# Kernel optimization log

Measured on AMD Instinct MI355X. Metric: run time of the kernel, lower is better.

Reference implementation:

```python
import jax, jax.numpy as jnp
import numpy as np

K = 3
STRIDE = 1
PAD = 1

def conv2d(x, w, b, stride, padding):
    out = jax.lax.conv_general_dilated(x, w, (stride, stride), [(padding, padding), (padding, padding)],
                                       dimension_numbers=('NCHW', 'OIHW', 'NCHW'))
    if b is not None:
        out = out + b[None, :, None, None]
    return out

def deform_conv2d(x, offset, mask, weight, stride, padding):
    # torchvision-style modulated deformable conv (offset_groups=1, groups=1)
    B, C, H, W = x.shape
    C2 = weight.shape[0]
    KK = K * K
    Hout, Wout = offset.shape[2], offset.shape[3]
    off = offset.reshape(B, KK, 2, Hout, Wout)  # (dy, dx) pairs per kernel tap
    ky = jnp.repeat(jnp.arange(K), K)  # kernel row per tap [KK]
    kx = jnp.tile(jnp.arange(K), K)    # kernel col per tap [KK]
    base_y = (jnp.arange(Hout) * stride - padding).astype(jnp.float32)
    base_x = (jnp.arange(Wout) * stride - padding).astype(jnp.float32)
    py = off[:, :, 0] + ky[None, :, None, None] + base_y[None, None, :, None]  # [B,KK,Hout,Wout]
    px = off[:, :, 1] + kx[None, :, None, None] + base_x[None, None, None, :]
    y0f = jnp.floor(py); x0f = jnp.floor(px)
    ly = py - y0f; lx = px - x0f
    y0 = y0f.astype(jnp.int32); x0 = x0f.astype(jnp.int32)
    xf = x.reshape(B, C, H * W)

    def corner(yi, xi, wgt):
        valid = (yi >= 0) & (yi < H) & (xi >= 0) & (xi < W)
        idx = (jnp.clip(yi, 0, H - 1) * W + jnp.clip(xi, 0, W - 1)).reshape(B, -1)  # [B, KK*Hout*Wout]
        v = jax.vmap(lambda xb, ib: xb[:, ib])(xf, idx)  # [B, C, KK*Hout*Wout]
        return v * (wgt * valid).reshape(B, 1, -1)

    val = (corner(y0, x0, (1.0 - ly) * (1.0 - lx))
           + corner(y0, x0 + 1, (1.0 - ly) * lx)
           + corner(y0 + 1, x0, ly * (1.0 - lx))
           + corner(y0 + 1, x0 + 1, ly * lx))
    val = val * mask.reshape(B, 1, -1)  # modulation per (tap, spatial)
    val = val.reshape(B, C, KK, Hout, Wout)
    out = jnp.einsum('bckhw,ock->bohw', val, weight.reshape(C2, C, KK))
    return out

def setup_inputs() -> dict:
    key = jax.random.key(0)
    ks = jax.random.split(key, 6)
    B, C1, C2, H, W = 8, 256, 256, 64, 64
    x = jax.random.normal(ks[0], (B, C1, H, W), jnp.float32)
    offset_w = jax.random.normal(ks[1], (2 * K * K, C1, K, K), jnp.float32) * 0.01
    offset_b = jax.random.normal(ks[2], (2 * K * K,), jnp.float32) * 0.5
    mod_w = jax.random.normal(ks[3], (K * K, C1, K, K), jnp.float32) * 0.01
    mod_b = jnp.zeros((K * K,), jnp.float32)
    reg_w = jax.random.normal(ks[4], (C2, C1, K, K), jnp.float32) * np.float32(1.0 / np.sqrt(C1 * K * K))
    return {"x": x, "offset_w": offset_w, "offset_b": offset_b, "mod_w": mod_w, "mod_b": mod_b, "reg_w": reg_w}

def reference(x, offset_w, offset_b, mod_w, mod_b, reg_w):
    h, w = x.shape[2], x.shape[3]
    max_offset = max(h, w) / 4.0
    offset = jnp.clip(conv2d(x, offset_w, offset_b, STRIDE, PAD), -max_offset, max_offset)
    modulator = jax.nn.sigmoid(conv2d(x, mod_w, mod_b, STRIDE, PAD))
    return deform_conv2d(x, offset, modulator, reg_w, STRIDE, PAD)
```

## Files before the change

### kernel.cpp

```cpp
#include <hip/hip_runtime.h>
#include <math.h>

#define BB 8
#define CIN 256
#define COUT 256
#define HH 64
#define WW 64
#define OCM 27
#define KTOT 2304
#define NKT 72

typedef unsigned int u32;
typedef unsigned short u16;
typedef _Float16 f16;

#define WS_XBF 0
#define WS_W2 16777216
#define WS_W2OM 17956864
#define WS_OFFMOD 18104320

__device__ __forceinline__ u16 f2h(float f) {
    f16 h = (f16)f;
    return __builtin_bit_cast(u16, h);
}

typedef __attribute__((address_space(1))) const unsigned int* gptr_t;
typedef __attribute__((address_space(3))) unsigned int* lptr_t;
__device__ __forceinline__ void gl2lds16(const void* g, void* l) {
    __builtin_amdgcn_global_load_lds((gptr_t)g, (lptr_t)l, 16, 0, 0);
}

typedef __attribute__((ext_vector_type(8))) f16 frag;
typedef __attribute__((ext_vector_type(2))) f16 h2;
typedef __attribute__((ext_vector_type(4))) float f4;

__device__ __forceinline__ int sw_off(int row, int oct) {
    return (row << 5) + ((oct ^ ((row >> 1) & 3)) << 3);
}

#define BARRIER_RAW() do { asm volatile("" ::: "memory"); \
    __builtin_amdgcn_s_barrier(); asm volatile("" ::: "memory"); } while (0)

__global__ __launch_bounds__(256) void k_prep(
    const float* __restrict__ x, const float* __restrict__ rw,
    const float* __restrict__ ow, const float* __restrict__ mw,
    u16* __restrict__ xbf, u16* __restrict__ w2, u16* __restrict__ w2om)
{
    const int bid = blockIdx.x;
    const int t = threadIdx.x;
    if (bid < 2048) {
        const int c0 = (bid & 3) << 6;
        const int y = (bid >> 2) & 63;
        const int b = bid >> 8;
        __shared__ float T[64][65];
        const int c = t >> 2, fi = t & 3;
        const float* xrow = x + (((size_t)(b * 256 + c0 + c)) << 12) + (y << 6);
#pragma unroll
        for (int k = 0; k < 4; ++k) {
            float4 v = *(const float4*)(xrow + ((fi + 4 * k) << 2));
            int w = (fi + 4 * k) << 2;
            T[c][w] = v.x; T[c][w + 1] = v.y; T[c][w + 2] = v.z; T[c][w + 3] = v.w;
        }
        __syncthreads();
        const int wl = t & 63, g = t >> 6;
        const int pr = wl & 31, wsub = wl >> 5;
        u32* xo = (u32*)xbf;
#pragma unroll
        for (int j = 0; j < 8; ++j) {
            int w = j * 8 + g * 2 + wsub;
            u32 v = (u32)f2h(T[2 * pr][w]) | ((u32)f2h(T[2 * pr + 1][w]) << 16);
            xo[((((size_t)b << 12) + (y << 6) + w) << 7) + (c0 >> 1) + pr] = v;
        }
    } else if (bid < 2336) {
        int o = ((bid - 2048) << 8) + t;
        int kk8 = (o & 3) << 3;
        int n = (o >> 2) & 255;
        int kt = o >> 10;
        u16 tmp[8];
#pragma unroll
        for (int j = 0; j < 8; ++j) {
            int k = kt * 32 + kk8 + j;
            int tap = k >> 8, c = k & 255;
            tmp[j] = f2h(rw[n * KTOT + c * 9 + tap]);
        }
        *(uint4*)&w2[((size_t)kt << 13) + (n << 5) + kk8] = *(uint4*)tmp;
    } else {
        int o = ((bid - 2336) << 8) + t;
        int kk8 = (o & 3) << 3;
        int oc = (o >> 2) & 31;
        int kt = o >> 7;
        u16 tmp[8];
#pragma unroll
        for (int j = 0; j < 8; ++j) {
            int k = kt * 32 + kk8 + j;
            int tap = k >> 8, c = k & 255;
            float v = 0.f;
            if (oc < 18) v = ow[oc * KTOT + c * 9 + tap];
            else if (oc < 27) v = mw[(oc - 18) * KTOT + c * 9 + tap];
            tmp[j] = f2h(v);
        }
        *(uint4*)&w2om[((size_t)kt << 10) + (oc << 5) + kk8] = *(uint4*)tmp;
    }
}

__global__ __launch_bounds__(512, 4) void k_offmod6(
    const u16* __restrict__ xbf, const u16* __restrict__ w2om,
    const float* __restrict__ ob, const float* __restrict__ mb,
    float* __restrict__ offmod)
{
    const int b = blockIdx.x & 7, h = blockIdx.x >> 3;
    const int t = threadIdx.x;
    const int lane = t & 63, wv = t >> 6;
    const int hf = wv >> 2;
    const int wl4 = wv & 3;
    const int th = t & 255;
    const int fr = lane & 15, q = lane >> 4;
    const int wm = wl4 << 4;
    const int mg = th >> 2, oct = th & 3;

    __shared__ u16 AsB[2][2][64 * 32];
    __shared__ u16 BsB[2][2][32 * 32];
    __shared__ float red[64][33];

    const u16* xb = xbf + ((size_t)b << 20);
    const int kbase = hf * 36;

    auto loadA = [&](int kt, uint4* r) {
        int tap = kt >> 3;
        int yy = h + tap / 3 - 1, xx = mg + tap % 3 - 1;
        int c0 = ((kt & 7) << 5) + (oct << 3);
        uint4 v = make_uint4(0, 0, 0, 0);
        if ((unsigned)yy < HH && (unsigned)xx < WW)
            v = *(const uint4*)(xb + (((size_t)yy << 6) + xx) * 256 + c0);
        *r = v;
    };
    auto loadB = [&](int kt, uint4* r) {
        if (th < 128) *r = *(const uint4*)(w2om + (size_t)kt * 1024 + (th >> 2) * 32 + (th & 3) * 8);
    };
    auto storeAB = [&](int buf, uint4* rA, uint4* rB) {
        *(uint4*)&AsB[hf][buf][sw_off(mg, oct)] = *rA;
        if (th < 128) *(uint4*)&BsB[hf][buf][sw_off(th >> 2, th & 3)] = *rB;
    };

    f4 acc[2];
    acc[0] = (f4){0.f, 0.f, 0.f, 0.f};
    acc[1] = (f4){0.f, 0.f, 0.f, 0.f};

    uint4 rA0, rB0, rA1, rB1;
    loadA(kbase, &rA0); loadB(kbase, &rB0);
    storeAB(0, &rA0, &rB0);
    loadA(kbase + 1, &rA1); loadB(kbase + 1, &rB1);
    asm volatile("s_waitcnt lgkmcnt(0)" ::: "memory");

    auto body = [&](int i, int p, uint4* cA, uint4* cB, uint4* nA, uint4* nB) {
        BARRIER_RAW();
        frag a  = *(const frag*)&AsB[hf][p][sw_off(wm + fr, q)];
        frag b0 = *(const frag*)&BsB[hf][p][sw_off(fr, q)];
        frag b1 = *(const frag*)&BsB[hf][p][sw_off(16 + fr, q)];
        if (i + 2 < 36) { loadA(kbase + i + 2, nA); loadB(kbase + i + 2, nB); }
        if (i + 1 < 36) storeAB(1 - p, cA, cB);
        acc[0] = __builtin_amdgcn_mfma_f32_16x16x32_f16(a, b0, acc[0], 0, 0, 0);
        acc[1] = __builtin_amdgcn_mfma_f32_16x16x32_f16(a, b1, acc[1], 0, 0, 0);
        asm volatile("s_waitcnt lgkmcnt(0)" ::: "memory");
    };
    for (int i = 0; i < 36; i += 2) {
        body(i, 0, &rA1, &rB1, &rA0, &rB0);
        body(i + 1, 1, &rA0, &rB0, &rA1, &rB1);
    }

    if (hf == 1) {
#pragma unroll
        for (int ni = 0; ni < 2; ++ni)
#pragma unroll
            for (int r = 0; r < 4; ++r)
                red[wm + q * 4 + r][ni * 16 + fr] = acc[ni][r];
    }
    __syncthreads();
    if (hf == 0) {
#pragma unroll
        for (int ni = 0; ni < 2; ++ni) {
            int oc = ni * 16 + fr;
            if (oc >= OCM) continue;
            bool is_off = oc < 18;
            float bias = is_off ? ob[oc] : mb[oc - 18];
            float4 v;
            float* vp = (float*)&v;
#pragma unroll
            for (int r = 0; r < 4; ++r) {
                float s = acc[ni][r] + red[wm + q * 4 + r][oc] + bias;
                vp[r] = is_off ? fminf(fmaxf(s, -16.f), 16.f)
                               : 1.f / (1.f + __expf(-s));
            }
            *(float4*)&offmod[(((size_t)b * OCM + oc) << 12) + (h << 6) + wm + q * 4] = v;
        }
    }
}

__global__ __launch_bounds__(1024, 4) void k_deform8(
    const u16* __restrict__ xbf, const float* __restrict__ offmod,
    const u16* __restrict__ w2, float* __restrict__ out)
{
    const int t = threadIdx.x;
    const int b = blockIdx.x & 7, hp = blockIdx.x >> 3;
    const int h0 = hp << 1;
    const int lane = t & 63, wv = t >> 6;

    __shared__ uint4 STAB[9][128];
    __shared__ u16 AsB[2][128 * 32];
    __shared__ u16 BsB[2][256 * 32];

    const float* om = offmod + (size_t)b * OCM * 4096;
    for (int e = t; e < 9 * 128; e += 1024) {
        int m = e & 127, tap = e >> 7;
        int hh = h0 + (m >> 6), ww = m & 63;
        float dy = om[(tap * 2) * 4096 + hh * 64 + ww];
        float dx = om[(tap * 2 + 1) * 4096 + hh * 64 + ww];
        float mv = om[(18 + tap) * 4096 + hh * 64 + ww];
        float py = dy + (float)(tap / 3) + (float)(hh - 1);
        float px = dx + (float)(tap % 3) + (float)(ww - 1);
        float y0f = floorf(py), x0f = floorf(px);
        float ly = py - y0f, lx = px - x0f;
        int y0 = (int)y0f, x0 = (int)x0f;
        int   ysr[2] = {y0, y0 + 1};
        int   xsr[2] = {x0, x0 + 1};
        float wy[2] = {1.f - ly, ly};
        float wx[2] = {1.f - lx, lx};
        u16 idx[4]; f16 wgt[4];
#pragma unroll
        for (int r = 0; r < 4; ++r) {
            int yy = ysr[r >> 1], xx = xsr[r & 1];
            bool ok = ((unsigned)yy < HH) && ((unsigned)xx < WW);
            int yc = min(max(yy, 0), HH - 1);
            int xc = min(max(xx, 0), WW - 1);
            idx[r] = (u16)(yc * WW + xc);
            wgt[r] = (f16)(ok ? (wy[r >> 1] * wx[r & 1] * mv) : 0.f);
        }
        uint4 tv;
        tv.x = (u32)idx[0] | ((u32)idx[1] << 16);
        tv.y = (u32)idx[2] | ((u32)idx[3] << 16);
        h2 w01 = {wgt[0], wgt[1]};
        h2 w23 = {wgt[2], wgt[3]};
        tv.z = __builtin_bit_cast(u32, w01);
        tv.w = __builtin_bit_cast(u32, w23);
        STAB[tap][m] = tv;
    }
    __syncthreads();

    if (wv < 8) {
        const int fr = lane & 15, q = lane >> 4;
        const int wn = wv << 5;

        f4 acc[8][2];
#pragma unroll
        for (int mi = 0; mi < 8; ++mi) {
            acc[mi][0] = (f4){0.f, 0.f, 0.f, 0.f};
            acc[mi][1] = (f4){0.f, 0.f, 0.f, 0.f};
        }

        for (int kt = 0; kt < NKT; ++kt) {
            const int p = kt & 1;
            BARRIER_RAW();
            frag b0 = *(const frag*)&BsB[p][sw_off(wn + fr, q)];
            frag b1 = *(const frag*)&BsB[p][sw_off(wn + 16 + fr, q)];
#pragma unroll
            for (int mi = 0; mi < 8; ++mi) {
                frag a = *(const frag*)&AsB[p][sw_off(mi * 16 + fr, q)];
                acc[mi][0] = __builtin_amdgcn_mfma_f32_16x16x32_f16(a, b0, acc[mi][0], 0, 0, 0);
                acc[mi][1] = __builtin_amdgcn_mfma_f32_16x16x32_f16(a, b1, acc[mi][1], 0, 0, 0);
            }
        }

#pragma unroll
        for (int ni = 0; ni < 2; ++ni) {
            int n_g = wn + ni * 16 + fr;
            float* outn = out + (((size_t)b * COUT + n_g) << 12) + (h0 << 6);
#pragma unroll
            for (int mi = 0; mi < 8; ++mi) {
                int off = ((mi >> 2) << 6) + ((mi & 3) << 4) + (q << 2);
                *(float4*)&outn[off] = make_float4(acc[mi][ni][0], acc[mi][ni][1],
                                                   acc[mi][ni][2], acc[mi][ni][3]);
            }
        }
    } else {
        const int pt = t - 512;
        const int mg = pt >> 2, oct = pt & 3;
        const int pwv = wv - 8;
        const int ko_sw = (lane & 3) ^ ((lane >> 3) & 3);
        const u16* xpl = xbf + ((size_t)b << 20);

        auto stageB = [&](int kt, int buf) {
            const u16* src = w2 + ((size_t)kt << 13);
#pragma unroll
            for (int j = 0; j < 2; ++j) {
                int base = (pwv << 5) + (j << 4);
                int n = base + (lane >> 2);
                u16* dst = &BsB[buf][base << 5];
                gl2lds16(src + n * 32 + ko_sw * 8, dst);
            }
        };
        auto loadCorners = [&](int kt, uint4 (&cr)[4]) {
            int tap = kt >> 3;
            int c0 = ((kt & 7) << 5) + (oct << 3);
            uint2 iv = *(const uint2*)&STAB[tap][mg];
            const u16* base = xpl + c0;
            cr[0] = *(const uint4*)(base + ((size_t)(iv.x & 0xFFFFu) << 8));
            cr[1] = *(const uint4*)(base + ((size_t)(iv.x >> 16) << 8));
            cr[2] = *(const uint4*)(base + ((size_t)(iv.y & 0xFFFFu) << 8));
            cr[3] = *(const uint4*)(base + ((size_t)(iv.y >> 16) << 8));
        };
        auto interpStore = [&](int kt, int buf, uint4 (&cr)[4]) {
            int tap = kt >> 3;
            uint2 wvp = *(const uint2*)(((const u32*)&STAB[tap][mg]) + 2);
            h2 w01 = __builtin_bit_cast(h2, wvp.x);
            h2 w23 = __builtin_bit_cast(h2, wvp.y);
            h2 s0 = {w01[0], w01[0]};
            h2 s1 = {w01[1], w01[1]};
            h2 s2 = {w23[0], w23[0]};
            h2 s3 = {w23[1], w23[1]};
            const u32* c0p = (const u32*)&cr[0];
            const u32* c1p = (const u32*)&cr[1];
            const u32* c2p = (const u32*)&cr[2];
            const u32* c3p = (const u32*)&cr[3];
            u32 o[4];
#pragma unroll
            for (int jj = 0; jj < 4; ++jj) {
                h2 v = s0 * __builtin_bit_cast(h2, c0p[jj]);
                v += s1 * __builtin_bit_cast(h2, c1p[jj]);
                v += s2 * __builtin_bit_cast(h2, c2p[jj]);
                v += s3 * __builtin_bit_cast(h2, c3p[jj]);
                o[jj] = __builtin_bit_cast(u32, v);
            }
            *(uint4*)&AsB[buf][sw_off(mg, oct)] = make_uint4(o[0], o[1], o[2], o[3]);
        };

        uint4 cr0[4], cr1[4], cr2[4];
        stageB(0, 0);
        loadCorners(0, cr0);
        loadCorners(1, cr1);
        loadCorners(2, cr2);
        interpStore(0, 0, cr0);
        asm volatile("s_waitcnt lgkmcnt(0)" ::: "memory");

        auto pstep = [&](int kt, int p, uint4 (&cur)[4], uint4 (&nxt)[4]) {
            if (kt + 2 < NKT) asm volatile("s_waitcnt vmcnt(4)" ::: "memory");
            else              asm volatile("s_waitcnt vmcnt(0)" ::: "memory");
            BARRIER_RAW();
            if (kt + 1 < NKT) stageB(kt + 1, 1 - p);
            if (kt + 3 < NKT) loadCorners(kt + 3, nxt);
            if (kt + 1 < NKT) interpStore(kt + 1, 1 - p, cur);
            asm volatile("s_waitcnt lgkmcnt(0)" ::: "memory");
        };
        for (int kt = 0; kt < NKT; kt += 6) {
            pstep(kt,     0, cr1, cr0);
            pstep(kt + 1, 1, cr2, cr1);
            pstep(kt + 2, 0, cr0, cr2);
            pstep(kt + 3, 1, cr1, cr0);
            pstep(kt + 4, 0, cr2, cr1);
            pstep(kt + 5, 1, cr0, cr2);
        }
    }
}

extern "C" void kernel_launch(void* const* d_in, const int* in_sizes, int n_in,
                              void* d_out, int out_size, void* d_ws, size_t ws_size,
                              hipStream_t stream) {
    const float* x  = (const float*)d_in[0];
    const float* ow = (const float*)d_in[1];
    const float* ob = (const float*)d_in[2];
    const float* mw = (const float*)d_in[3];
    const float* mb = (const float*)d_in[4];
    const float* rw = (const float*)d_in[5];
    float* out = (float*)d_out;
    char* ws = (char*)d_ws;

    u16*   xbf    = (u16*)(ws + WS_XBF);
    u16*   w2     = (u16*)(ws + WS_W2);
    u16*   w2om   = (u16*)(ws + WS_W2OM);
    float* offmod = (float*)(ws + WS_OFFMOD);

    k_prep<<<dim3(2372), 256, 0, stream>>>(x, rw, ow, mw, xbf, w2, w2om);
    k_offmod6<<<dim3(512), 512, 0, stream>>>(xbf, w2om, ob, mb, offmod);
    k_deform8<<<dim3(256), 1024, 0, stream>>>(xbf, offmod, w2, out);
}
```

Baseline: 166.4 us.

## Load weight fragments directly from global into registers and retile MFMA waves 2x4

The B (weight) operand no longer goes through LDS via producer-staged loads. Each consumer wave now reads its weight fragments straight from global memory into registers, double-buffered across k-steps. Waves are retiled from 8 waves × 32 output channels × 128 pixels to a 2×4 grid of 64 pixels × 64 channels, which cuts A-fragment LDS reads per MFMA. This frees LDS and producer work, but weight reads now depend on L2/L1 hits, and global load latency sits closer to the MFMA loop.

```diff
diff --git a/kernel.cpp b/kernel.cpp
--- a/kernel.cpp
+++ b/kernel.cpp
@@ -196,7 +196,7 @@
     }
 }
 
-__global__ __launch_bounds__(1024, 4) void k_deform8(
+__global__ __launch_bounds__(1024, 4) void k_deform10(
     const u16* __restrict__ xbf, const float* __restrict__ offmod,
     const u16* __restrict__ w2, float* __restrict__ out)
 {
@@ -207,7 +207,6 @@
 
     __shared__ uint4 STAB[9][128];
     __shared__ u16 AsB[2][128 * 32];
-    __shared__ u16 BsB[2][256 * 32];
 
     const float* om = offmod + (size_t)b * OCM * 4096;
     for (int e = t; e < 9 * 128; e += 1024) {
@@ -248,56 +247,76 @@
 
     if (wv < 8) {
         const int fr = lane & 15, q = lane >> 4;
-        const int wn = wv << 5;
-
-        f4 acc[8][2];
-#pragma unroll
-        for (int mi = 0; mi < 8; ++mi) {
-            acc[mi][0] = (f4){0.f, 0.f, 0.f, 0.f};
-            acc[mi][1] = (f4){0.f, 0.f, 0.f, 0.f};
-        }
-
-        for (int kt = 0; kt < NKT; ++kt) {
-            const int p = kt & 1;
+        const int wn4 = wv & 3;
+        const int wm2 = wv >> 2;
+        const u16* w2n = w2 + ((wn4 << 6) + fr) * 32 + q * 8;
+
+        f4 acc[4][4];
+#pragma unroll
+        for (int mi = 0; mi < 4; ++mi)
+#pragma unroll
+            for (int ni = 0; ni < 4; ++ni) acc[mi][ni] = (f4){0.f, 0.f, 0.f, 0.f};
+
+        uint4 bA[4], bB[4];
+#pragma unroll
+        for (int ni = 0; ni < 4; ++ni)
+            bA[ni] = *(const uint4*)(w2n + ni * 512);
+
+        for (int kt = 0; kt < NKT; kt += 2) {
             BARRIER_RAW();
-            frag b0 = *(const frag*)&BsB[p][sw_off(wn + fr, q)];
-            frag b1 = *(const frag*)&BsB[p][sw_off(wn + 16 + fr, q)];
-#pragma unroll
-            for (int mi = 0; mi < 8; ++mi) {
-                frag a = *(const frag*)&AsB[p][sw_off(mi * 16 + fr, q)];
-                acc[mi][0] = __builtin_amdgcn_mfma_f32_16x16x32_f16(a, b0, acc[mi][0], 0, 0, 0);
-                acc[mi][1] = __builtin_amdgcn_mfma_f32_16x16x32_f16(a, b1, acc[mi][1], 0, 0, 0);
+            {
+                frag av[4];
+#pragma unroll
+                for (int mi = 0; mi < 4; ++mi)
+                    av[mi] = *(const frag*)&AsB[0][sw_off((wm2 << 6) + mi * 16 + fr, q)];
+                const u16* src = w2n + (size_t)(kt + 1) * 8192;
+#pragma unroll
+                for (int ni = 0; ni < 4; ++ni)
+                    bB[ni] = *(const uint4*)(src + ni * 512);
+#pragma unroll
+                for (int mi = 0; mi < 4; ++mi)
+#pragma unroll
+                    for (int ni = 0; ni < 4; ++ni)
+                        acc[mi][ni] = __builtin_amdgcn_mfma_f32_16x16x32_f16(
+                            av[mi], __builtin_bit_cast(frag, bA[ni]), acc[mi][ni], 0, 0, 0);
             }
-        }
-
-#pragma unroll
-        for (int ni = 0; ni < 2; ++ni) {
-            int n_g = wn + ni * 16 + fr;
-            float* outn = out + (((size_t)b * COUT + n_g) << 12) + (h0 << 6);
-#pragma unroll
-            for (int mi = 0; mi < 8; ++mi) {
-                int off = ((mi >> 2) << 6) + ((mi & 3) << 4) + (q << 2);
-                *(float4*)&outn[off] = make_float4(acc[mi][ni][0], acc[mi][ni][1],
-                                                   acc[mi][ni][2], acc[mi][ni][3]);
+            BARRIER_RAW();
+            {
+                frag av[4];
+#pragma unroll
+                for (int mi = 0; mi < 4; ++mi)
+                    av[mi] = *(const frag*)&AsB[1][sw_off((wm2 << 6) + mi * 16 + fr, q)];
+                if (kt + 2 < NKT) {
+                    const u16* src = w2n + (size_t)(kt + 2) * 8192;
+#pragma unroll
+                    for (int ni = 0; ni < 4; ++ni)
+                        bA[ni] = *(const uint4*)(src + ni * 512);
+                }
+#pragma unroll
+                for (int mi = 0; mi < 4; ++mi)
+#pragma unroll
+                    for (int ni = 0; ni < 4; ++ni)
+                        acc[mi][ni] = __builtin_amdgcn_mfma_f32_16x16x32_f16(
+                            av[mi], __builtin_bit_cast(frag, bB[ni]), acc[mi][ni], 0, 0, 0);
+            }
+        }
+
+#pragma unroll
+        for (int ni = 0; ni < 4; ++ni) {
+            int n_g = (wn4 << 6) + ni * 16 + fr;
+            float* outn = out + (((size_t)b * COUT + n_g) << 12) + ((h0 + wm2) << 6);
+#pragma unroll
+            for (int mi = 0; mi < 4; ++mi) {
+                *(float4*)&outn[mi * 16 + (q << 2)] =
+                    make_float4(acc[mi][ni][0], acc[mi][ni][1],
+                                acc[mi][ni][2], acc[mi][ni][3]);
             }
         }
     } else {
         const int pt = t - 512;
         const int mg = pt >> 2, oct = pt & 3;
-        const int pwv = wv - 8;
-        const int ko_sw = (lane & 3) ^ ((lane >> 3) & 3);
         const u16* xpl = xbf + ((size_t)b << 20);
 
-        auto stageB = [&](int kt, int buf) {
-            const u16* src = w2 + ((size_t)kt << 13);
-#pragma unroll
-            for (int j = 0; j < 2; ++j) {
-                int base = (pwv << 5) + (j << 4);
-                int n = base + (lane >> 2);
-                u16* dst = &BsB[buf][base << 5];
-                gl2lds16(src + n * 32 + ko_sw * 8, dst);
-            }
-        };
         auto loadCorners = [&](int kt, uint4 (&cr)[4]) {
             int tap = kt >> 3;
             int c0 = ((kt & 7) << 5) + (oct << 3);
@@ -334,7 +353,6 @@
         };
 
         uint4 cr0[4], cr1[4], cr2[4];
-        stageB(0, 0);
         loadCorners(0, cr0);
         loadCorners(1, cr1);
         loadCorners(2, cr2);
@@ -345,7 +363,6 @@
             if (kt + 2 < NKT) asm volatile("s_waitcnt vmcnt(4)" ::: "memory");
             else              asm volatile("s_waitcnt vmcnt(0)" ::: "memory");
             BARRIER_RAW();
-            if (kt + 1 < NKT) stageB(kt + 1, 1 - p);
             if (kt + 3 < NKT) loadCorners(kt + 3, nxt);
             if (kt + 1 < NKT) interpStore(kt + 1, 1 - p, cur);
             asm volatile("s_waitcnt lgkmcnt(0)" ::: "memory");
@@ -380,5 +397,5 @@
 
     k_prep<<<dim3(2372), 256, 0, stream>>>(x, rw, ow, mw, xbf, w2, w2om);
     k_offmod6<<<dim3(512), 512, 0, stream>>>(xbf, w2om, ob, mb, offmod);
-    k_deform8<<<dim3(256), 1024, 0, stream>>>(xbf, offmod, w2, out);
-}
+    k_deform10<<<dim3(256), 1024, 0, stream>>>(xbf, offmod, w2, out);
+}
```

Result: slower. 216.2 us (+29.9%).

## Load weight fragments directly into registers instead of staging through LDS

Applied to the files above, without the earlier changes.

The MFMA waves now read their B (weight) fragments straight from global memory into registers, double-buffered one k-step ahead, instead of having producer waves copy them into a shared LDS buffer. This removes the BsB shared array, the producer-side weight staging, and the LDS reads of B, which frees LDS and lowers LDS traffic. In exchange each consumer wave issues global loads whose latency must be hidden behind one k-step of MFMAs. Weight tiles are also no longer shared through LDS, so L2 traffic for weights rises.

```diff
diff --git a/kernel.cpp b/kernel.cpp
--- a/kernel.cpp
+++ b/kernel.cpp
@@ -196,7 +196,7 @@
     }
 }
 
-__global__ __launch_bounds__(1024, 4) void k_deform8(
+__global__ __launch_bounds__(1024, 4) void k_deform11(
     const u16* __restrict__ xbf, const float* __restrict__ offmod,
     const u16* __restrict__ w2, float* __restrict__ out)
 {
@@ -207,7 +207,6 @@
 
     __shared__ uint4 STAB[9][128];
     __shared__ u16 AsB[2][128 * 32];
-    __shared__ u16 BsB[2][256 * 32];
 
     const float* om = offmod + (size_t)b * OCM * 4096;
     for (int e = t; e < 9 * 128; e += 1024) {
@@ -249,6 +248,7 @@
     if (wv < 8) {
         const int fr = lane & 15, q = lane >> 4;
         const int wn = wv << 5;
+        const u16* w2n = w2 + ((wn + fr) << 5) + (q << 3);
 
         f4 acc[8][2];
 #pragma unroll
@@ -257,16 +257,40 @@
             acc[mi][1] = (f4){0.f, 0.f, 0.f, 0.f};
         }
 
-        for (int kt = 0; kt < NKT; ++kt) {
-            const int p = kt & 1;
+        uint4 bA0, bA1, bB0, bB1;
+        bA0 = *(const uint4*)(w2n);
+        bA1 = *(const uint4*)(w2n + 512);
+
+        for (int kt = 0; kt < NKT; kt += 2) {
             BARRIER_RAW();
-            frag b0 = *(const frag*)&BsB[p][sw_off(wn + fr, q)];
-            frag b1 = *(const frag*)&BsB[p][sw_off(wn + 16 + fr, q)];
-#pragma unroll
-            for (int mi = 0; mi < 8; ++mi) {
-                frag a = *(const frag*)&AsB[p][sw_off(mi * 16 + fr, q)];
-                acc[mi][0] = __builtin_amdgcn_mfma_f32_16x16x32_f16(a, b0, acc[mi][0], 0, 0, 0);
-                acc[mi][1] = __builtin_amdgcn_mfma_f32_16x16x32_f16(a, b1, acc[mi][1], 0, 0, 0);
+            {
+                const u16* src = w2n + (size_t)(kt + 1) * 8192;
+                bB0 = *(const uint4*)(src);
+                bB1 = *(const uint4*)(src + 512);
+                frag fb0 = __builtin_bit_cast(frag, bA0);
+                frag fb1 = __builtin_bit_cast(frag, bA1);
+#pragma unroll
+                for (int mi = 0; mi < 8; ++mi) {
+                    frag a = *(const frag*)&AsB[0][sw_off(mi * 16 + fr, q)];
+                    acc[mi][0] = __builtin_amdgcn_mfma_f32_16x16x32_f16(a, fb0, acc[mi][0], 0, 0, 0);
+                    acc[mi][1] = __builtin_amdgcn_mfma_f32_16x16x32_f16(a, fb1, acc[mi][1], 0, 0, 0);
+                }
+            }
+            BARRIER_RAW();
+            {
+                if (kt + 2 < NKT) {
+                    const u16* src = w2n + (size_t)(kt + 2) * 8192;
+                    bA0 = *(const uint4*)(src);
+                    bA1 = *(const uint4*)(src + 512);
+                }
+                frag fb0 = __builtin_bit_cast(frag, bB0);
+                frag fb1 = __builtin_bit_cast(frag, bB1);
+#pragma unroll
+                for (int mi = 0; mi < 8; ++mi) {
+                    frag a = *(const frag*)&AsB[1][sw_off(mi * 16 + fr, q)];
+                    acc[mi][0] = __builtin_amdgcn_mfma_f32_16x16x32_f16(a, fb0, acc[mi][0], 0, 0, 0);
+                    acc[mi][1] = __builtin_amdgcn_mfma_f32_16x16x32_f16(a, fb1, acc[mi][1], 0, 0, 0);
+                }
             }
         }
 
@@ -284,20 +308,8 @@
     } else {
         const int pt = t - 512;
         const int mg = pt >> 2, oct = pt & 3;
-        const int pwv = wv - 8;
-        const int ko_sw = (lane & 3) ^ ((lane >> 3) & 3);
         const u16* xpl = xbf + ((size_t)b << 20);
 
-        auto stageB = [&](int kt, int buf) {
-            const u16* src = w2 + ((size_t)kt << 13);
-#pragma unroll
-            for (int j = 0; j < 2; ++j) {
-                int base = (pwv << 5) + (j << 4);
-                int n = base + (lane >> 2);
-                u16* dst = &BsB[buf][base << 5];
-                gl2lds16(src + n * 32 + ko_sw * 8, dst);
-            }
-        };
         auto loadCorners = [&](int kt, uint4 (&cr)[4]) {
             int tap = kt >> 3;
             int c0 = ((kt & 7) << 5) + (oct << 3);
@@ -334,7 +346,6 @@
         };
 
         uint4 cr0[4], cr1[4], cr2[4];
-        stageB(0, 0);
         loadCorners(0, cr0);
         loadCorners(1, cr1);
         loadCorners(2, cr2);
@@ -345,7 +356,6 @@
             if (kt + 2 < NKT) asm volatile("s_waitcnt vmcnt(4)" ::: "memory");
             else              asm volatile("s_waitcnt vmcnt(0)" ::: "memory");
             BARRIER_RAW();
-            if (kt + 1 < NKT) stageB(kt + 1, 1 - p);
             if (kt + 3 < NKT) loadCorners(kt + 3, nxt);
             if (kt + 1 < NKT) interpStore(kt + 1, 1 - p, cur);
             asm volatile("s_waitcnt lgkmcnt(0)" ::: "memory");
@@ -380,5 +390,5 @@
 
     k_prep<<<dim3(2372), 256, 0, stream>>>(x, rw, ow, mw, xbf, w2, w2om);
     k_offmod6<<<dim3(512), 512, 0, stream>>>(xbf, w2om, ob, mb, offmod);
-    k_deform8<<<dim3(256), 1024, 0, stream>>>(xbf, offmod, w2, out);
-}
+    k_deform11<<<dim3(256), 1024, 0, stream>>>(xbf, offmod, w2, out);
+}
```

Measured after the change: 167.6 us. About the same (+0.7%).
